# Kernel optimization log

Hardware: AMD Instinct MI355X
Metric: run time of the kernel (lower is better)

The kernel has to match this reference:

```python
import jax, jax.numpy as jnp
import numpy as np

N_NODES = 100000
N_EDGES = 1600000
NFEAT = 256
NHID = 128


def _l2_normalize(v, eps=1e-12):
    return v / (jnp.linalg.norm(v) + eps)


def setup_inputs() -> dict:
    key = jax.random.key(0)
    k1, k2, k3, k4 = jax.random.split(key, 4)
    x = jax.random.normal(k1, (N_NODES, NFEAT), dtype=jnp.float32)
    edge_index = jax.random.randint(k2, (2, N_EDGES), 0, N_NODES, dtype=jnp.int64)
    # GCNConv weight (glorot-ish scale), spectral-normalized at forward time
    W = jax.random.normal(k3, (NFEAT, NHID), dtype=jnp.float32) * 0.05
    bias = jnp.zeros((NHID,), dtype=jnp.float32)
    prelu_a = jnp.full((1,), 0.25, dtype=jnp.float32)  # nn.PReLU default slope
    u = _l2_normalize(jax.random.normal(k4, (NFEAT,), dtype=jnp.float32))
    return {"x": x, "edge_index": edge_index, "W": W, "bias": bias,
            "prelu_a": prelu_a, "u": u}


def reference(x, edge_index, W, bias, prelu_a, u):
    # --- spectral_norm: one power iteration (torch default n_power_iterations=1) ---
    v = _l2_normalize(W.T @ u)          # [NHID]
    u2 = _l2_normalize(W @ v)           # [NFEAT]
    sigma = u2 @ (W @ v)
    W_sn = W / sigma

    # --- GCNConv: linear transform, add self-loops, sym-normalize, scatter-add ---
    xw = x @ W_sn                       # [N, NHID]
    n = x.shape[0]
    loops = jnp.arange(n, dtype=edge_index.dtype)
    row = jnp.concatenate([edge_index[0], loops])  # sources
    col = jnp.concatenate([edge_index[1], loops])  # targets
    ones = jnp.ones(row.shape[0], dtype=x.dtype)
    deg = jax.ops.segment_sum(ones, col, num_segments=n)
    dinv = jnp.where(deg > 0, deg ** -0.5, 0.0)
    norm = dinv[row] * dinv[col]        # [E+N]
    msgs = norm[:, None] * xw[row]      # gather at sources
    out = jax.ops.segment_sum(msgs, col, num_segments=n) + bias

    # --- PReLU ---
    return jnp.where(out > 0, out, prelu_a * out)
```

## Files before the change

### kernel.cpp

```cpp
#include <hip/hip_runtime.h>

#define NFEAT 256
#define NHID  128

#define NBK   391
#define EPB   4096
#define NBLK  391

typedef __bf16 bf16x8 __attribute__((ext_vector_type(8)));
typedef __bf16 bf16x4 __attribute__((ext_vector_type(4)));
typedef float  f32x4  __attribute__((ext_vector_type(4)));

__global__ __launch_bounds__(256) void sigma_kernel(const float* __restrict__ W,
                                                    const float* __restrict__ u,
                                                    float* __restrict__ scal) {
    __shared__ float v[NHID];
    __shared__ float red[256];
    int tid = threadIdx.x;

    float t = 0.f;
    if (tid < NHID) {
        for (int i = 0; i < NFEAT; ++i) t += W[i * NHID + tid] * u[i];
    }
    red[tid] = (tid < NHID) ? t * t : 0.f;
    __syncthreads();
    for (int s = 128; s > 0; s >>= 1) {
        if (tid < s) red[tid] += red[tid + s];
        __syncthreads();
    }
    float nv = sqrtf(red[0]);
    float inv_nv = 1.f / (nv + 1e-12f);
    __syncthreads();
    if (tid < NHID) v[tid] = t * inv_nv;
    __syncthreads();

    float wv = 0.f;
    for (int j = 0; j < NHID; ++j) wv += W[tid * NHID + j] * v[j];
    red[tid] = wv * wv;
    __syncthreads();
    for (int s = 128; s > 0; s >>= 1) {
        if (tid < s) red[tid] += red[tid + s];
        __syncthreads();
    }
    if (tid == 0) {
        float n2  = red[0];
        float nwv = sqrtf(n2);
        float sigma = n2 / (nwv + 1e-12f);
        scal[0] = 1.f / sigma;
    }
}

__global__ __launch_bounds__(256) void wt_kernel(const float* __restrict__ W,
                                                 const float* __restrict__ scal,
                                                 __bf16* __restrict__ WT) {
    int idx = blockIdx.x * 256 + threadIdx.x;
    int c = idx >> 8;
    int r = idx & 255;
    WT[c * NFEAT + r] = (__bf16)(W[r * NHID + c] * scal[0]);
}

__global__ __launch_bounds__(256) void hist_kernel(const int* __restrict__ ecol,
                                                   int* __restrict__ blkhist, int E) {
    __shared__ int hist[NBK];
    int tid = threadIdx.x, b = blockIdx.x;
    for (int k = tid; k < NBK; k += 256) hist[k] = 0;
    __syncthreads();
    int e0 = b * EPB;
#pragma unroll
    for (int j = 0; j < 16; ++j) {
        int idx = e0 + j * 256 + tid;
        if (idx < E) atomicAdd(&hist[ecol[idx] >> 8], 1);
    }
    __syncthreads();
    for (int k = tid; k < NBK; k += 256) blkhist[k * NBLK + b] = hist[k];
}

__global__ __launch_bounds__(256) void scan_rows_kernel(int* __restrict__ blkhist,
                                                        int* __restrict__ btot) {
    int k = blockIdx.x * 4 + (threadIdx.x >> 6);
    int lane = threadIdx.x & 63;
    if (k >= NBK) return;
    int carry = 0;
    for (int c0 = 0; c0 < NBLK; c0 += 64) {
        int b = c0 + lane;
        int v = (b < NBLK) ? blkhist[k * NBLK + b] : 0;
        int orig = v;
#pragma unroll
        for (int d = 1; d < 64; d <<= 1) {
            int t = __shfl_up(v, (unsigned)d, 64);
            if (lane >= d) v += t;
        }
        if (b < NBLK) blkhist[k * NBLK + b] = carry + v - orig;
        carry += __shfl(v, 63, 64);
    }
    if (lane == 0) btot[k] = carry;
}

__global__ __launch_bounds__(512) void scan_buckets_kernel(const int* __restrict__ btot,
                                                           int* __restrict__ bbase) {
    __shared__ int s[512];
    int tid = threadIdx.x;
    int v = (tid < NBK) ? btot[tid] : 0;
    s[tid] = v;
    __syncthreads();
    int val = v;
    for (int off = 1; off < 512; off <<= 1) {
        int t = (tid >= off) ? s[tid - off] : 0;
        __syncthreads();
        val += t;
        s[tid] = val;
        __syncthreads();
    }
    if (tid <= NBK) bbase[tid] = val - v;
}

__global__ __launch_bounds__(512) void coarse_scatter_kernel(const int* __restrict__ erow,
                                                             const int* __restrict__ ecol,
                                                             const int* __restrict__ blkhist,
                                                             const int* __restrict__ bbase,
                                                             unsigned int* __restrict__ rbuf,
                                                             int E) {
    __shared__ unsigned int rec[EPB];
    __shared__ unsigned short bk[EPB];
    __shared__ int hist[NBK], sc[512], lbase[NBK], lfill[NBK], gb[NBK];
    int tid = threadIdx.x, b = blockIdx.x;
    for (int k = tid; k < NBK; k += 512) { hist[k] = 0; lfill[k] = 0; }
    __syncthreads();
    int e0 = b * EPB;
    unsigned int rv[8];
    int kv[8];
#pragma unroll
    for (int j = 0; j < 8; ++j) {
        int idx = e0 + j * 512 + tid;
        if (idx < E) {
            int c = ecol[idx];
            int s = erow[idx];
            int k = c >> 8;
            kv[j] = k;
            rv[j] = ((unsigned int)(c & 255) << 24) | (unsigned int)s;
            atomicAdd(&hist[k], 1);
        } else kv[j] = -1;
    }
    __syncthreads();
    int hv = (tid < NBK) ? hist[tid] : 0;
    sc[tid] = hv;
    __syncthreads();
    int val = hv;
    for (int off = 1; off < 512; off <<= 1) {
        int t = (tid >= off) ? sc[tid - off] : 0;
        __syncthreads();
        val += t;
        sc[tid] = val;
        __syncthreads();
    }
    if (tid < NBK) {
        lbase[tid] = val - hv;
        gb[tid] = bbase[tid] + blkhist[tid * NBLK + b];
    }
    __syncthreads();
#pragma unroll
    for (int j = 0; j < 8; ++j) {
        if (kv[j] >= 0) {
            int p = lbase[kv[j]] + atomicAdd(&lfill[kv[j]], 1);
            rec[p] = rv[j];
            bk[p] = (unsigned short)kv[j];
        }
    }
    __syncthreads();
    int nval = E - e0;
    if (nval > EPB) nval = EPB;
    for (int p = tid; p < nval; p += 512) {
        int k = bk[p];
        rbuf[gb[k] + (p - lbase[k])] = rec[p];
    }
}

__global__ __launch_bounds__(256) void fine_kernel(const unsigned int* __restrict__ rbuf,
                                                   const int* __restrict__ bbase,
                                                   int* __restrict__ base_g,
                                                   int* __restrict__ cnt_g,
                                                   float* __restrict__ dinv,
                                                   int* __restrict__ ebuf, int n) {
    __shared__ int cnt[256], lb[256], lf[256], sc[256];
    int tid = threadIdx.x, k = blockIdx.x;
    int seg0 = bbase[k], seg1 = bbase[k + 1];
    cnt[tid] = 0;
    lf[tid] = 0;
    __syncthreads();
    for (int j = seg0 + tid; j < seg1; j += 256)
        atomicAdd(&cnt[rbuf[j] >> 24], 1);
    __syncthreads();
    int cv = cnt[tid];
    sc[tid] = cv;
    __syncthreads();
    int val = cv;
    for (int off = 1; off < 256; off <<= 1) {
        int t = (tid >= off) ? sc[tid - off] : 0;
        __syncthreads();
        val += t;
        sc[tid] = val;
        __syncthreads();
    }
    lb[tid] = val - cv;
    __syncthreads();
    int node = k * 256 + tid;
    if (node < n) {
        base_g[node] = seg0 + lb[tid];
        cnt_g[node] = cv;
        dinv[node] = rsqrtf((float)cv + 1.f);
    }
    for (int j = seg0 + tid; j < seg1; j += 256) {
        unsigned int r = rbuf[j];
        int dl = r >> 24;
        int p = seg0 + lb[dl] + atomicAdd(&lf[dl], 1);
        ebuf[p] = (int)(r & 0xFFFFFFu);
    }
}

__global__ __launch_bounds__(256) void gemm_mfma_kernel(const float* __restrict__ x,
                                                        const __bf16* __restrict__ WT,
                                                        const float* __restrict__ dinv,
                                                        __bf16* __restrict__ xwb, int nn) {
    __shared__ float xs[2][64][64];

    int tid  = threadIdx.x;
    int lane = tid & 63;
    int w    = tid >> 6;
    int rfrag = lane & 15;
    int kg    = lane >> 4;
    int row0 = blockIdx.x * 64;

    int p16  = lane & 15;
    int rsub = lane >> 4;

    int crow0 = (w & 1) * 32 + rfrag;
    int col0  = (w >> 1) * 64;
    int r0 = row0 + crow0;
    int r1 = r0 + 16;
    const __bf16* wb = WT + (size_t)(col0 + rfrag) * NFEAT + kg * 8;
    int cr7 = crow0 & 7;

    f32x4 acc0[4] = {};
    f32x4 acc1[4] = {};

    auto STAGE = [&](int buf, int c) {
#pragma unroll
        for (int j = 0; j < 4; ++j) {
            int rloc = w * 16 + j * 4 + rsub;
            int grow = row0 + rloc;
            if (grow >= nn) grow = nn - 1;
            const float* src = x + (size_t)grow * NFEAT + c * 64 + ((p16 ^ (grow & 7)) << 2);
            __builtin_amdgcn_global_load_lds(
                (const __attribute__((address_space(1))) void*)src,
                (__attribute__((address_space(3))) void*)&xs[buf][w * 16 + j * 4][0],
                16, 0, 0);
        }
    };

    bf16x8 Bf[2][4];
    auto BLOAD = [&](int c) {
#pragma unroll
        for (int ks = 0; ks < 2; ++ks)
#pragma unroll
            for (int nt = 0; nt < 4; ++nt)
                Bf[ks][nt] = *(const bf16x8*)(wb + (size_t)nt * 16 * NFEAT + c * 64 + ks * 32);
    };

    auto MFMA_CHUNK = [&](int buf) {
#pragma unroll
        for (int ks = 0; ks < 2; ++ks) {
            int sA = kg * 2 + ks * 8;
            float4 a0lo = *(const float4*)&xs[buf][crow0][((sA) ^ cr7) * 4];
            float4 a0hi = *(const float4*)&xs[buf][crow0][((sA + 1) ^ cr7) * 4];
            float4 a1lo = *(const float4*)&xs[buf][crow0 + 16][((sA) ^ cr7) * 4];
            float4 a1hi = *(const float4*)&xs[buf][crow0 + 16][((sA + 1) ^ cr7) * 4];
            bf16x8 af0, af1;
            af0[0] = (__bf16)a0lo.x; af0[1] = (__bf16)a0lo.y;
            af0[2] = (__bf16)a0lo.z; af0[3] = (__bf16)a0lo.w;
            af0[4] = (__bf16)a0hi.x; af0[5] = (__bf16)a0hi.y;
            af0[6] = (__bf16)a0hi.z; af0[7] = (__bf16)a0hi.w;
            af1[0] = (__bf16)a1lo.x; af1[1] = (__bf16)a1lo.y;
            af1[2] = (__bf16)a1lo.z; af1[3] = (__bf16)a1lo.w;
            af1[4] = (__bf16)a1hi.x; af1[5] = (__bf16)a1hi.y;
            af1[6] = (__bf16)a1hi.z; af1[7] = (__bf16)a1hi.w;
#pragma unroll
            for (int nt = 0; nt < 4; ++nt) {
                acc0[nt] = __builtin_amdgcn_mfma_f32_16x16x32_bf16(Bf[ks][nt], af0, acc0[nt], 0, 0, 0);
                acc1[nt] = __builtin_amdgcn_mfma_f32_16x16x32_bf16(Bf[ks][nt], af1, acc1[nt], 0, 0, 0);
            }
        }
    };

#define DRAIN_BAR() do { \
        asm volatile("s_waitcnt vmcnt(0)" ::: "memory"); \
        __builtin_amdgcn_s_barrier(); } while (0)

    STAGE(0, 0);
    DRAIN_BAR();

    BLOAD(0);
    __builtin_amdgcn_sched_barrier(0);
    STAGE(1, 1);
    __builtin_amdgcn_sched_barrier(0);
    MFMA_CHUNK(0);
    DRAIN_BAR();

    BLOAD(1);
    __builtin_amdgcn_sched_barrier(0);
    STAGE(0, 2);
    __builtin_amdgcn_sched_barrier(0);
    MFMA_CHUNK(1);
    DRAIN_BAR();

    BLOAD(2);
    __builtin_amdgcn_sched_barrier(0);
    STAGE(1, 3);
    __builtin_amdgcn_sched_barrier(0);
    MFMA_CHUNK(0);
    DRAIN_BAR();

    BLOAD(3);
    MFMA_CHUNK(1);
#undef DRAIN_BAR

    if (r0 < nn) {
        float d = dinv[r0];
        __bf16* orow = xwb + (size_t)r0 * NHID + col0 + kg * 4;
#pragma unroll
        for (int nt = 0; nt < 4; ++nt) {
            bf16x4 v;
            v[0] = (__bf16)(acc0[nt][0] * d);
            v[1] = (__bf16)(acc0[nt][1] * d);
            v[2] = (__bf16)(acc0[nt][2] * d);
            v[3] = (__bf16)(acc0[nt][3] * d);
            *(bf16x4*)&orow[nt * 16] = v;
        }
    }
    if (r1 < nn) {
        float d = dinv[r1];
        __bf16* orow = xwb + (size_t)r1 * NHID + col0 + kg * 4;
#pragma unroll
        for (int nt = 0; nt < 4; ++nt) {
            bf16x4 v;
            v[0] = (__bf16)(acc1[nt][0] * d);
            v[1] = (__bf16)(acc1[nt][1] * d);
            v[2] = (__bf16)(acc1[nt][2] * d);
            v[3] = (__bf16)(acc1[nt][3] * d);
            *(bf16x4*)&orow[nt * 16] = v;
        }
    }
}

__global__ __launch_bounds__(256) void gather_kernel(const uint4* __restrict__ xb4,
                                                     const int* __restrict__ base,
                                                     const int* __restrict__ cnt,
                                                     const int* __restrict__ ebuf,
                                                     const float* __restrict__ dinv,
                                                     const float* __restrict__ bias,
                                                     const float* __restrict__ pa,
                                                     float* __restrict__ out, int n) {
    int tid = threadIdx.x;
    int sub = tid & 15;
    int node = (blockIdx.x * 256 + tid) >> 4;
    if (node >= n) return;

    int b = base[node];
    int deg = cnt[node];

    uint4 s0 = xb4[(size_t)node * 16 + sub];
    float a0 = __uint_as_float(s0.x << 16);
    float a1 = __uint_as_float(s0.x & 0xffff0000u);
    float a2 = __uint_as_float(s0.y << 16);
    float a3 = __uint_as_float(s0.y & 0xffff0000u);
    float a4 = __uint_as_float(s0.z << 16);
    float a5 = __uint_as_float(s0.z & 0xffff0000u);
    float a6 = __uint_as_float(s0.w << 16);
    float a7 = __uint_as_float(s0.w & 0xffff0000u);

    int k = 0;
    for (; k + 4 <= deg; k += 4) {
        int r0 = ebuf[b + k + 0];
        int r1 = ebuf[b + k + 1];
        int r2 = ebuf[b + k + 2];
        int r3 = ebuf[b + k + 3];
        uint4 v0 = xb4[(size_t)r0 * 16 + sub];
        uint4 v1 = xb4[(size_t)r1 * 16 + sub];
        uint4 v2 = xb4[(size_t)r2 * 16 + sub];
        uint4 v3 = xb4[(size_t)r3 * 16 + sub];
        a0 += __uint_as_float(v0.x << 16) + __uint_as_float(v1.x << 16)
            + __uint_as_float(v2.x << 16) + __uint_as_float(v3.x << 16);
        a1 += __uint_as_float(v0.x & 0xffff0000u) + __uint_as_float(v1.x & 0xffff0000u)
            + __uint_as_float(v2.x & 0xffff0000u) + __uint_as_float(v3.x & 0xffff0000u);
        a2 += __uint_as_float(v0.y << 16) + __uint_as_float(v1.y << 16)
            + __uint_as_float(v2.y << 16) + __uint_as_float(v3.y << 16);
        a3 += __uint_as_float(v0.y & 0xffff0000u) + __uint_as_float(v1.y & 0xffff0000u)
            + __uint_as_float(v2.y & 0xffff0000u) + __uint_as_float(v3.y & 0xffff0000u);
        a4 += __uint_as_float(v0.z << 16) + __uint_as_float(v1.z << 16)
            + __uint_as_float(v2.z << 16) + __uint_as_float(v3.z << 16);
        a5 += __uint_as_float(v0.z & 0xffff0000u) + __uint_as_float(v1.z & 0xffff0000u)
            + __uint_as_float(v2.z & 0xffff0000u) + __uint_as_float(v3.z & 0xffff0000u);
        a6 += __uint_as_float(v0.w << 16) + __uint_as_float(v1.w << 16)
            + __uint_as_float(v2.w << 16) + __uint_as_float(v3.w << 16);
        a7 += __uint_as_float(v0.w & 0xffff0000u) + __uint_as_float(v1.w & 0xffff0000u)
            + __uint_as_float(v2.w & 0xffff0000u) + __uint_as_float(v3.w & 0xffff0000u);
    }
    for (; k < deg; ++k) {
        int r = ebuf[b + k];
        uint4 v = xb4[(size_t)r * 16 + sub];
        a0 += __uint_as_float(v.x << 16);
        a1 += __uint_as_float(v.x & 0xffff0000u);
        a2 += __uint_as_float(v.y << 16);
        a3 += __uint_as_float(v.y & 0xffff0000u);
        a4 += __uint_as_float(v.z << 16);
        a5 += __uint_as_float(v.z & 0xffff0000u);
        a6 += __uint_as_float(v.w << 16);
        a7 += __uint_as_float(v.w & 0xffff0000u);
    }

    float s = dinv[node];
    float alpha = pa[0];
    const float4* bb4 = (const float4*)bias;
    float4 b0 = bb4[sub * 2], b1 = bb4[sub * 2 + 1];
    float o0 = s * a0 + b0.x;
    float o1 = s * a1 + b0.y;
    float o2 = s * a2 + b0.z;
    float o3 = s * a3 + b0.w;
    float o4 = s * a4 + b1.x;
    float o5 = s * a5 + b1.y;
    float o6 = s * a6 + b1.z;
    float o7 = s * a7 + b1.w;
    o0 = o0 > 0.f ? o0 : alpha * o0;
    o1 = o1 > 0.f ? o1 : alpha * o1;
    o2 = o2 > 0.f ? o2 : alpha * o2;
    o3 = o3 > 0.f ? o3 : alpha * o3;
    o4 = o4 > 0.f ? o4 : alpha * o4;
    o5 = o5 > 0.f ? o5 : alpha * o5;
    o6 = o6 > 0.f ? o6 : alpha * o6;
    o7 = o7 > 0.f ? o7 : alpha * o7;
    float4* orow = (float4*)out + (size_t)node * 32 + sub * 2;
    orow[0] = make_float4(o0, o1, o2, o3);
    orow[1] = make_float4(o4, o5, o6, o7);
}

extern "C" void kernel_launch(void* const* d_in, const int* in_sizes, int n_in,
                              void* d_out, int out_size, void* d_ws, size_t ws_size,
                              hipStream_t stream) {
    const float* x    = (const float*)d_in[0];
    const int*   ei   = (const int*)d_in[1];
    const float* W    = (const float*)d_in[2];
    const float* bias = (const float*)d_in[3];
    const float* pa   = (const float*)d_in[4];
    const float* u    = (const float*)d_in[5];

    int n = in_sizes[0] / NFEAT;
    int e = in_sizes[1] / 2;
    const int* erow = ei;
    const int* ecol = ei + e;

    float* out = (float*)d_out;
    char* ws = (char*)d_ws;
    float*        scal   = (float*)(ws);
    int*          btot   = (int*)  (ws + 0x0001000);
    int*          bbase  = (int*)  (ws + 0x0002000);
    __bf16*       WT     = (__bf16*)(ws + 0x0010000);
    int*          base_g = (int*)  (ws + 0x0100000);
    int*          cnt_g  = (int*)  (ws + 0x0200000);
    float*        dinv   = (float*)(ws + 0x0300000);
    int*          blkhist= (int*)  (ws + 0x0400000);
    unsigned int* rbuf   = (unsigned int*)(ws + 0x0500000);
    int*          ebuf   = (int*)  (ws + 0x0C00000);
    __bf16*       xwb    = (__bf16*)(ws + 0x1300000);

    sigma_kernel<<<1, 256, 0, stream>>>(W, u, scal);
    wt_kernel<<<(NFEAT * NHID) / 256, 256, 0, stream>>>(W, scal, WT);

    hist_kernel<<<NBLK, 256, 0, stream>>>(ecol, blkhist, e);
    scan_rows_kernel<<<(NBK + 3) / 4, 256, 0, stream>>>(blkhist, btot);
    scan_buckets_kernel<<<1, 512, 0, stream>>>(btot, bbase);
    coarse_scatter_kernel<<<NBLK, 512, 0, stream>>>(erow, ecol, blkhist, bbase, rbuf, e);
    fine_kernel<<<NBK, 256, 0, stream>>>(rbuf, bbase, base_g, cnt_g, dinv, ebuf, n);

    gemm_mfma_kernel<<<(n + 63) / 64, 256, 0, stream>>>(x, WT, dinv, xwb, n);

    long long gunits = (long long)n * 16;
    gather_kernel<<<(int)((gunits + 255) / 256), 256, 0, stream>>>(
        (const uint4*)xwb, base_g, cnt_g, ebuf, dinv, bias, pa, out, n);
}
```

Before: 157.3 us.

## Fuse GEMM with coarse edge scatter and use fixed-stride atomic bucket segments

Removes the global histogram, row scan and bucket scan kernels by giving each bucket a fixed-capacity segment (SEGW) whose fill level is claimed with a global atomicAdd. The coarse scatter now runs in the same launch as the MFMA GEMM, with blocks split by index, so the two independent stages overlap. Because dinv is no longer known when the GEMM runs, the per-source degree scaling moves into the gather, which adds an extra dinv load per edge. The fixed segment size assumes no bucket holds more than SEGW edges, which holds only for roughly uniform column distributions, and edge order within a bucket becomes nondeterministic.

New measurement: 146.1 us. 1.08x faster.

```diff
diff --git a/kernel.cpp b/kernel.cpp
--- a/kernel.cpp
+++ b/kernel.cpp
@@ -6,6 +6,7 @@
 #define NBK   391
 #define EPB   4096
 #define NBLK  391
+#define SEGW  4608
 
 typedef __bf16 bf16x8 __attribute__((ext_vector_type(8)));
 typedef __bf16 bf16x4 __attribute__((ext_vector_type(4)));
@@ -13,10 +14,14 @@
 
 __global__ __launch_bounds__(256) void sigma_kernel(const float* __restrict__ W,
                                                     const float* __restrict__ u,
-                                                    float* __restrict__ scal) {
+                                                    float* __restrict__ scal,
+                                                    int* __restrict__ bucket_fill) {
     __shared__ float v[NHID];
     __shared__ float red[256];
     int tid = threadIdx.x;
+
+    if (tid < NBK) bucket_fill[tid] = 0;
+    if (tid + 256 < NBK) bucket_fill[tid + 256] = 0;
 
     float t = 0.f;
     if (tid < NHID) {
@@ -59,79 +64,164 @@
     WT[c * NFEAT + r] = (__bf16)(W[r * NHID + c] * scal[0]);
 }
 
-__global__ __launch_bounds__(256) void hist_kernel(const int* __restrict__ ecol,
-                                                   int* __restrict__ blkhist, int E) {
-    __shared__ int hist[NBK];
-    int tid = threadIdx.x, b = blockIdx.x;
-    for (int k = tid; k < NBK; k += 256) hist[k] = 0;
-    __syncthreads();
+__global__ __launch_bounds__(256) void fused_kernel(const float* __restrict__ x,
+                                                    const __bf16* __restrict__ WT,
+                                                    __bf16* __restrict__ xwb,
+                                                    const int* __restrict__ erow,
+                                                    const int* __restrict__ ecol,
+                                                    int* __restrict__ bucket_fill,
+                                                    unsigned int* __restrict__ rbuf,
+                                                    int nn, int E, int ngemm) {
+    __shared__ __attribute__((aligned(16))) char sbuf[32768];
+
+    int tid  = threadIdx.x;
+
+    if ((int)blockIdx.x < ngemm) {
+        float (*xs)[64][64] = (float (*)[64][64])sbuf;
+
+        int lane = tid & 63;
+        int w    = tid >> 6;
+        int rfrag = lane & 15;
+        int kg    = lane >> 4;
+        int row0 = blockIdx.x * 64;
+
+        int p16  = lane & 15;
+        int rsub = lane >> 4;
+
+        int crow0 = (w & 1) * 32 + rfrag;
+        int col0  = (w >> 1) * 64;
+        int r0 = row0 + crow0;
+        int r1 = r0 + 16;
+        const __bf16* wb = WT + (size_t)(col0 + rfrag) * NFEAT + kg * 8;
+        int cr7 = crow0 & 7;
+
+        f32x4 acc0[4] = {};
+        f32x4 acc1[4] = {};
+
+        auto STAGE = [&](int buf, int c) {
+#pragma unroll
+            for (int j = 0; j < 4; ++j) {
+                int rloc = w * 16 + j * 4 + rsub;
+                int grow = row0 + rloc;
+                if (grow >= nn) grow = nn - 1;
+                const float* src = x + (size_t)grow * NFEAT + c * 64 + ((p16 ^ (grow & 7)) << 2);
+                __builtin_amdgcn_global_load_lds(
+                    (const __attribute__((address_space(1))) void*)src,
+                    (__attribute__((address_space(3))) void*)&xs[buf][w * 16 + j * 4][0],
+                    16, 0, 0);
+            }
+        };
+
+        bf16x8 Bf[2][4];
+        auto BLOAD = [&](int c) {
+#pragma unroll
+            for (int ks = 0; ks < 2; ++ks)
+#pragma unroll
+                for (int nt = 0; nt < 4; ++nt)
+                    Bf[ks][nt] = *(const bf16x8*)(wb + (size_t)nt * 16 * NFEAT + c * 64 + ks * 32);
+        };
+
+        auto MFMA_CHUNK = [&](int buf) {
+#pragma unroll
+            for (int ks = 0; ks < 2; ++ks) {
+                int sA = kg * 2 + ks * 8;
+                float4 a0lo = *(const float4*)&xs[buf][crow0][((sA) ^ cr7) * 4];
+                float4 a0hi = *(const float4*)&xs[buf][crow0][((sA + 1) ^ cr7) * 4];
+                float4 a1lo = *(const float4*)&xs[buf][crow0 + 16][((sA) ^ cr7) * 4];
+                float4 a1hi = *(const float4*)&xs[buf][crow0 + 16][((sA + 1) ^ cr7) * 4];
+                bf16x8 af0, af1;
+                af0[0] = (__bf16)a0lo.x; af0[1] = (__bf16)a0lo.y;
+                af0[2] = (__bf16)a0lo.z; af0[3] = (__bf16)a0lo.w;
+                af0[4] = (__bf16)a0hi.x; af0[5] = (__bf16)a0hi.y;
+                af0[6] = (__bf16)a0hi.z; af0[7] = (__bf16)a0hi.w;
+                af1[0] = (__bf16)a1lo.x; af1[1] = (__bf16)a1lo.y;
+                af1[2] = (__bf16)a1lo.z; af1[3] = (__bf16)a1lo.w;
+                af1[4] = (__bf16)a1hi.x; af1[5] = (__bf16)a1hi.y;
+                af1[6] = (__bf16)a1hi.z; af1[7] = (__bf16)a1hi.w;
+#pragma unroll
+                for (int nt = 0; nt < 4; ++nt) {
+                    acc0[nt] = __builtin_amdgcn_mfma_f32_16x16x32_bf16(Bf[ks][nt], af0, acc0[nt], 0, 0, 0);
+                    acc1[nt] = __builtin_amdgcn_mfma_f32_16x16x32_bf16(Bf[ks][nt], af1, acc1[nt], 0, 0, 0);
+                }
+            }
+        };
+
+#define DRAIN_BAR() do { \
+            asm volatile("s_waitcnt vmcnt(0)" ::: "memory"); \
+            __builtin_amdgcn_s_barrier(); } while (0)
+
+        STAGE(0, 0);
+        DRAIN_BAR();
+
+        BLOAD(0);
+        __builtin_amdgcn_sched_barrier(0);
+        STAGE(1, 1);
+        __builtin_amdgcn_sched_barrier(0);
+        MFMA_CHUNK(0);
+        DRAIN_BAR();
+
+        BLOAD(1);
+        __builtin_amdgcn_sched_barrier(0);
+        STAGE(0, 2);
+        __builtin_amdgcn_sched_barrier(0);
+        MFMA_CHUNK(1);
+        DRAIN_BAR();
+
+        BLOAD(2);
+        __builtin_amdgcn_sched_barrier(0);
+        STAGE(1, 3);
+        __builtin_amdgcn_sched_barrier(0);
+        MFMA_CHUNK(0);
+        DRAIN_BAR();
+
+        BLOAD(3);
+        MFMA_CHUNK(1);
+#undef DRAIN_BAR
+
+        if (r0 < nn) {
+            __bf16* orow = xwb + (size_t)r0 * NHID + col0 + kg * 4;
+#pragma unroll
+            for (int nt = 0; nt < 4; ++nt) {
+                bf16x4 v;
+                v[0] = (__bf16)acc0[nt][0];
+                v[1] = (__bf16)acc0[nt][1];
+                v[2] = (__bf16)acc0[nt][2];
+                v[3] = (__bf16)acc0[nt][3];
+                *(bf16x4*)&orow[nt * 16] = v;
+            }
+        }
+        if (r1 < nn) {
+            __bf16* orow = xwb + (size_t)r1 * NHID + col0 + kg * 4;
+#pragma unroll
+            for (int nt = 0; nt < 4; ++nt) {
+                bf16x4 v;
+                v[0] = (__bf16)acc1[nt][0];
+                v[1] = (__bf16)acc1[nt][1];
+                v[2] = (__bf16)acc1[nt][2];
+                v[3] = (__bf16)acc1[nt][3];
+                *(bf16x4*)&orow[nt * 16] = v;
+            }
+        }
+        return;
+    }
+
+    unsigned int*   rec   = (unsigned int*)sbuf;
+    unsigned short* bkk   = (unsigned short*)(sbuf + 16384);
+    int*            hist  = (int*)(sbuf + 24576);
+    int*            lbase = (int*)(sbuf + 24576 + 1564);
+    int*            lfill = (int*)(sbuf + 24576 + 3128);
+    int*            gb    = (int*)(sbuf + 24576 + 4692);
+
+    int b = blockIdx.x - ngemm;
+    for (int k = tid; k < NBK; k += 256) { hist[k] = 0; lfill[k] = 0; }
+    __syncthreads();
+
     int e0 = b * EPB;
+    unsigned int rv[16];
+    int kv[16];
 #pragma unroll
     for (int j = 0; j < 16; ++j) {
         int idx = e0 + j * 256 + tid;
-        if (idx < E) atomicAdd(&hist[ecol[idx] >> 8], 1);
-    }
-    __syncthreads();
-    for (int k = tid; k < NBK; k += 256) blkhist[k * NBLK + b] = hist[k];
-}
-
-__global__ __launch_bounds__(256) void scan_rows_kernel(int* __restrict__ blkhist,
-                                                        int* __restrict__ btot) {
-    int k = blockIdx.x * 4 + (threadIdx.x >> 6);
-    int lane = threadIdx.x & 63;
-    if (k >= NBK) return;
-    int carry = 0;
-    for (int c0 = 0; c0 < NBLK; c0 += 64) {
-        int b = c0 + lane;
-        int v = (b < NBLK) ? blkhist[k * NBLK + b] : 0;
-        int orig = v;
-#pragma unroll
-        for (int d = 1; d < 64; d <<= 1) {
-            int t = __shfl_up(v, (unsigned)d, 64);
-            if (lane >= d) v += t;
-        }
-        if (b < NBLK) blkhist[k * NBLK + b] = carry + v - orig;
-        carry += __shfl(v, 63, 64);
-    }
-    if (lane == 0) btot[k] = carry;
-}
-
-__global__ __launch_bounds__(512) void scan_buckets_kernel(const int* __restrict__ btot,
-                                                           int* __restrict__ bbase) {
-    __shared__ int s[512];
-    int tid = threadIdx.x;
-    int v = (tid < NBK) ? btot[tid] : 0;
-    s[tid] = v;
-    __syncthreads();
-    int val = v;
-    for (int off = 1; off < 512; off <<= 1) {
-        int t = (tid >= off) ? s[tid - off] : 0;
-        __syncthreads();
-        val += t;
-        s[tid] = val;
-        __syncthreads();
-    }
-    if (tid <= NBK) bbase[tid] = val - v;
-}
-
-__global__ __launch_bounds__(512) void coarse_scatter_kernel(const int* __restrict__ erow,
-                                                             const int* __restrict__ ecol,
-                                                             const int* __restrict__ blkhist,
-                                                             const int* __restrict__ bbase,
-                                                             unsigned int* __restrict__ rbuf,
-                                                             int E) {
-    __shared__ unsigned int rec[EPB];
-    __shared__ unsigned short bk[EPB];
-    __shared__ int hist[NBK], sc[512], lbase[NBK], lfill[NBK], gb[NBK];
-    int tid = threadIdx.x, b = blockIdx.x;
-    for (int k = tid; k < NBK; k += 512) { hist[k] = 0; lfill[k] = 0; }
-    __syncthreads();
-    int e0 = b * EPB;
-    unsigned int rv[8];
-    int kv[8];
-#pragma unroll
-    for (int j = 0; j < 8; ++j) {
-        int idx = e0 + j * 512 + tid;
         if (idx < E) {
             int c = ecol[idx];
             int s = erow[idx];
@@ -142,48 +232,56 @@
         } else kv[j] = -1;
     }
     __syncthreads();
-    int hv = (tid < NBK) ? hist[tid] : 0;
-    sc[tid] = hv;
-    __syncthreads();
-    int val = hv;
-    for (int off = 1; off < 512; off <<= 1) {
-        int t = (tid >= off) ? sc[tid - off] : 0;
-        __syncthreads();
-        val += t;
-        sc[tid] = val;
-        __syncthreads();
-    }
-    if (tid < NBK) {
-        lbase[tid] = val - hv;
-        gb[tid] = bbase[tid] + blkhist[tid * NBLK + b];
-    }
-    __syncthreads();
-#pragma unroll
-    for (int j = 0; j < 8; ++j) {
+
+    if (tid < 64) {
+        int carry = 0;
+        for (int c0 = 0; c0 < NBK; c0 += 64) {
+            int i = c0 + tid;
+            int vv = (i < NBK) ? hist[i] : 0;
+            int orig = vv;
+#pragma unroll
+            for (int d = 1; d < 64; d <<= 1) {
+                int t = __shfl_up(vv, (unsigned)d, 64);
+                if (tid >= d) vv += t;
+            }
+            if (i < NBK) lbase[i] = carry + vv - orig;
+            carry += __shfl(vv, 63, 64);
+        }
+    }
+    __syncthreads();
+
+    if (tid < NBK) gb[tid] = tid * SEGW + atomicAdd(&bucket_fill[tid], hist[tid]);
+    if (tid + 256 < NBK) gb[tid + 256] = (tid + 256) * SEGW
+                                       + atomicAdd(&bucket_fill[tid + 256], hist[tid + 256]);
+    __syncthreads();
+
+#pragma unroll
+    for (int j = 0; j < 16; ++j) {
         if (kv[j] >= 0) {
             int p = lbase[kv[j]] + atomicAdd(&lfill[kv[j]], 1);
             rec[p] = rv[j];
-            bk[p] = (unsigned short)kv[j];
+            bkk[p] = (unsigned short)kv[j];
         }
     }
     __syncthreads();
+
     int nval = E - e0;
     if (nval > EPB) nval = EPB;
-    for (int p = tid; p < nval; p += 512) {
-        int k = bk[p];
+    for (int p = tid; p < nval; p += 256) {
+        int k = bkk[p];
         rbuf[gb[k] + (p - lbase[k])] = rec[p];
     }
 }
 
 __global__ __launch_bounds__(256) void fine_kernel(const unsigned int* __restrict__ rbuf,
-                                                   const int* __restrict__ bbase,
+                                                   const int* __restrict__ bucket_fill,
                                                    int* __restrict__ base_g,
                                                    int* __restrict__ cnt_g,
                                                    float* __restrict__ dinv,
                                                    int* __restrict__ ebuf, int n) {
     __shared__ int cnt[256], lb[256], lf[256], sc[256];
     int tid = threadIdx.x, k = blockIdx.x;
-    int seg0 = bbase[k], seg1 = bbase[k + 1];
+    int seg0 = k * SEGW, seg1 = seg0 + bucket_fill[k];
     cnt[tid] = 0;
     lf[tid] = 0;
     __syncthreads();
@@ -214,140 +312,6 @@
         int dl = r >> 24;
         int p = seg0 + lb[dl] + atomicAdd(&lf[dl], 1);
         ebuf[p] = (int)(r & 0xFFFFFFu);
-    }
-}
-
-__global__ __launch_bounds__(256) void gemm_mfma_kernel(const float* __restrict__ x,
-                                                        const __bf16* __restrict__ WT,
-                                                        const float* __restrict__ dinv,
-                                                        __bf16* __restrict__ xwb, int nn) {
-    __shared__ float xs[2][64][64];
-
-    int tid  = threadIdx.x;
-    int lane = tid & 63;
-    int w    = tid >> 6;
-    int rfrag = lane & 15;
-    int kg    = lane >> 4;
-    int row0 = blockIdx.x * 64;
-
-    int p16  = lane & 15;
-    int rsub = lane >> 4;
-
-    int crow0 = (w & 1) * 32 + rfrag;
-    int col0  = (w >> 1) * 64;
-    int r0 = row0 + crow0;
-    int r1 = r0 + 16;
-    const __bf16* wb = WT + (size_t)(col0 + rfrag) * NFEAT + kg * 8;
-    int cr7 = crow0 & 7;
-
-    f32x4 acc0[4] = {};
-    f32x4 acc1[4] = {};
-
-    auto STAGE = [&](int buf, int c) {
-#pragma unroll
-        for (int j = 0; j < 4; ++j) {
-            int rloc = w * 16 + j * 4 + rsub;
-            int grow = row0 + rloc;
-            if (grow >= nn) grow = nn - 1;
-            const float* src = x + (size_t)grow * NFEAT + c * 64 + ((p16 ^ (grow & 7)) << 2);
-            __builtin_amdgcn_global_load_lds(
-                (const __attribute__((address_space(1))) void*)src,
-                (__attribute__((address_space(3))) void*)&xs[buf][w * 16 + j * 4][0],
-                16, 0, 0);
-        }
-    };
-
-    bf16x8 Bf[2][4];
-    auto BLOAD = [&](int c) {
-#pragma unroll
-        for (int ks = 0; ks < 2; ++ks)
-#pragma unroll
-            for (int nt = 0; nt < 4; ++nt)
-                Bf[ks][nt] = *(const bf16x8*)(wb + (size_t)nt * 16 * NFEAT + c * 64 + ks * 32);
-    };
-
-    auto MFMA_CHUNK = [&](int buf) {
-#pragma unroll
-        for (int ks = 0; ks < 2; ++ks) {
-            int sA = kg * 2 + ks * 8;
-            float4 a0lo = *(const float4*)&xs[buf][crow0][((sA) ^ cr7) * 4];
-            float4 a0hi = *(const float4*)&xs[buf][crow0][((sA + 1) ^ cr7) * 4];
-            float4 a1lo = *(const float4*)&xs[buf][crow0 + 16][((sA) ^ cr7) * 4];
-            float4 a1hi = *(const float4*)&xs[buf][crow0 + 16][((sA + 1) ^ cr7) * 4];
-            bf16x8 af0, af1;
-            af0[0] = (__bf16)a0lo.x; af0[1] = (__bf16)a0lo.y;
-            af0[2] = (__bf16)a0lo.z; af0[3] = (__bf16)a0lo.w;
-            af0[4] = (__bf16)a0hi.x; af0[5] = (__bf16)a0hi.y;
-            af0[6] = (__bf16)a0hi.z; af0[7] = (__bf16)a0hi.w;
-            af1[0] = (__bf16)a1lo.x; af1[1] = (__bf16)a1lo.y;
-            af1[2] = (__bf16)a1lo.z; af1[3] = (__bf16)a1lo.w;
-            af1[4] = (__bf16)a1hi.x; af1[5] = (__bf16)a1hi.y;
-            af1[6] = (__bf16)a1hi.z; af1[7] = (__bf16)a1hi.w;
-#pragma unroll
-            for (int nt = 0; nt < 4; ++nt) {
-                acc0[nt] = __builtin_amdgcn_mfma_f32_16x16x32_bf16(Bf[ks][nt], af0, acc0[nt], 0, 0, 0);
-                acc1[nt] = __builtin_amdgcn_mfma_f32_16x16x32_bf16(Bf[ks][nt], af1, acc1[nt], 0, 0, 0);
-            }
-        }
-    };
-
-#define DRAIN_BAR() do { \
-        asm volatile("s_waitcnt vmcnt(0)" ::: "memory"); \
-        __builtin_amdgcn_s_barrier(); } while (0)
-
-    STAGE(0, 0);
-    DRAIN_BAR();
-
-    BLOAD(0);
-    __builtin_amdgcn_sched_barrier(0);
-    STAGE(1, 1);
-    __builtin_amdgcn_sched_barrier(0);
-    MFMA_CHUNK(0);
-    DRAIN_BAR();
-
-    BLOAD(1);
-    __builtin_amdgcn_sched_barrier(0);
-    STAGE(0, 2);
-    __builtin_amdgcn_sched_barrier(0);
-    MFMA_CHUNK(1);
-    DRAIN_BAR();
-
-    BLOAD(2);
-    __builtin_amdgcn_sched_barrier(0);
-    STAGE(1, 3);
-    __builtin_amdgcn_sched_barrier(0);
-    MFMA_CHUNK(0);
-    DRAIN_BAR();
-
-    BLOAD(3);
-    MFMA_CHUNK(1);
-#undef DRAIN_BAR
-
-    if (r0 < nn) {
-        float d = dinv[r0];
-        __bf16* orow = xwb + (size_t)r0 * NHID + col0 + kg * 4;
-#pragma unroll
-        for (int nt = 0; nt < 4; ++nt) {
-            bf16x4 v;
-            v[0] = (__bf16)(acc0[nt][0] * d);
-            v[1] = (__bf16)(acc0[nt][1] * d);
-            v[2] = (__bf16)(acc0[nt][2] * d);
-            v[3] = (__bf16)(acc0[nt][3] * d);
-            *(bf16x4*)&orow[nt * 16] = v;
-        }
-    }
-    if (r1 < nn) {
-        float d = dinv[r1];
-        __bf16* orow = xwb + (size_t)r1 * NHID + col0 + kg * 4;
-#pragma unroll
-        for (int nt = 0; nt < 4; ++nt) {
-            bf16x4 v;
-            v[0] = (__bf16)(acc1[nt][0] * d);
-            v[1] = (__bf16)(acc1[nt][1] * d);
-            v[2] = (__bf16)(acc1[nt][2] * d);
-            v[3] = (__bf16)(acc1[nt][3] * d);
-            *(bf16x4*)&orow[nt * 16] = v;
-        }
     }
 }
 
@@ -366,16 +330,17 @@
 
     int b = base[node];
     int deg = cnt[node];
+    float dn = dinv[node];
 
     uint4 s0 = xb4[(size_t)node * 16 + sub];
-    float a0 = __uint_as_float(s0.x << 16);
-    float a1 = __uint_as_float(s0.x & 0xffff0000u);
-    float a2 = __uint_as_float(s0.y << 16);
-    float a3 = __uint_as_float(s0.y & 0xffff0000u);
-    float a4 = __uint_as_float(s0.z << 16);
-    float a5 = __uint_as_float(s0.z & 0xffff0000u);
-    float a6 = __uint_as_float(s0.w << 16);
-    float a7 = __uint_as_float(s0.w & 0xffff0000u);
+    float a0 = dn * __uint_as_float(s0.x << 16);
+    float a1 = dn * __uint_as_float(s0.x & 0xffff0000u);
+    float a2 = dn * __uint_as_float(s0.y << 16);
+    float a3 = dn * __uint_as_float(s0.y & 0xffff0000u);
+    float a4 = dn * __uint_as_float(s0.z << 16);
+    float a5 = dn * __uint_as_float(s0.z & 0xffff0000u);
+    float a6 = dn * __uint_as_float(s0.w << 16);
+    float a7 = dn * __uint_as_float(s0.w & 0xffff0000u);
 
     int k = 0;
     for (; k + 4 <= deg; k += 4) {
@@ -383,52 +348,53 @@
         int r1 = ebuf[b + k + 1];
         int r2 = ebuf[b + k + 2];
         int r3 = ebuf[b + k + 3];
+        float d0 = dinv[r0], d1 = dinv[r1], d2 = dinv[r2], d3 = dinv[r3];
         uint4 v0 = xb4[(size_t)r0 * 16 + sub];
         uint4 v1 = xb4[(size_t)r1 * 16 + sub];
         uint4 v2 = xb4[(size_t)r2 * 16 + sub];
         uint4 v3 = xb4[(size_t)r3 * 16 + sub];
-        a0 += __uint_as_float(v0.x << 16) + __uint_as_float(v1.x << 16)
-            + __uint_as_float(v2.x << 16) + __uint_as_float(v3.x << 16);
-        a1 += __uint_as_float(v0.x & 0xffff0000u) + __uint_as_float(v1.x & 0xffff0000u)
-            + __uint_as_float(v2.x & 0xffff0000u) + __uint_as_float(v3.x & 0xffff0000u);
-        a2 += __uint_as_float(v0.y << 16) + __uint_as_float(v1.y << 16)
-            + __uint_as_float(v2.y << 16) + __uint_as_float(v3.y << 16);
-        a3 += __uint_as_float(v0.y & 0xffff0000u) + __uint_as_float(v1.y & 0xffff0000u)
-            + __uint_as_float(v2.y & 0xffff0000u) + __uint_as_float(v3.y & 0xffff0000u);
-        a4 += __uint_as_float(v0.z << 16) + __uint_as_float(v1.z << 16)
-            + __uint_as_float(v2.z << 16) + __uint_as_float(v3.z << 16);
-        a5 += __uint_as_float(v0.z & 0xffff0000u) + __uint_as_float(v1.z & 0xffff0000u)
-            + __uint_as_float(v2.z & 0xffff0000u) + __uint_as_float(v3.z & 0xffff0000u);
-        a6 += __uint_as_float(v0.w << 16) + __uint_as_float(v1.w << 16)
-            + __uint_as_float(v2.w << 16) + __uint_as_float(v3.w << 16);
-        a7 += __uint_as_float(v0.w & 0xffff0000u) + __uint_as_float(v1.w & 0xffff0000u)
-            + __uint_as_float(v2.w & 0xffff0000u) + __uint_as_float(v3.w & 0xffff0000u);
+        a0 += d0 * __uint_as_float(v0.x << 16) + d1 * __uint_as_float(v1.x << 16)
+            + d2 * __uint_as_float(v2.x << 16) + d3 * __uint_as_float(v3.x << 16);
+        a1 += d0 * __uint_as_float(v0.x & 0xffff0000u) + d1 * __uint_as_float(v1.x & 0xffff0000u)
+            + d2 * __uint_as_float(v2.x & 0xffff0000u) + d3 * __uint_as_float(v3.x & 0xffff0000u);
+        a2 += d0 * __uint_as_float(v0.y << 16) + d1 * __uint_as_float(v1.y << 16)
+            + d2 * __uint_as_float(v2.y << 16) + d3 * __uint_as_float(v3.y << 16);
+        a3 += d0 * __uint_as_float(v0.y & 0xffff0000u) + d1 * __uint_as_float(v1.y & 0xffff0000u)
+            + d2 * __uint_as_float(v2.y & 0xffff0000u) + d3 * __uint_as_float(v3.y & 0xffff0000u);
+        a4 += d0 * __uint_as_float(v0.z << 16) + d1 * __uint_as_float(v1.z << 16)
+            + d2 * __uint_as_float(v2.z << 16) + d3 * __uint_as_float(v3.z << 16);
+        a5 += d0 * __uint_as_float(v0.z & 0xffff0000u) + d1 * __uint_as_float(v1.z & 0xffff0000u)
+            + d2 * __uint_as_float(v2.z & 0xffff0000u) + d3 * __uint_as_float(v3.z & 0xffff0000u);
+        a6 += d0 * __uint_as_float(v0.w << 16) + d1 * __uint_as_float(v1.w << 16)
+            + d2 * __uint_as_float(v2.w << 16) + d3 * __uint_as_float(v3.w << 16);
+        a7 += d0 * __uint_as_float(v0.w & 0xffff0000u) + d1 * __uint_as_float(v1.w & 0xffff0000u)
+            + d2 * __uint_as_float(v2.w & 0xffff0000u) + d3 * __uint_as_float(v3.w & 0xffff0000u);
     }
     for (; k < deg; ++k) {
         int r = ebuf[b + k];
+        float d = dinv[r];
         uint4 v = xb4[(size_t)r * 16 + sub];
-        a0 += __uint_as_float(v.x << 16);
-        a1 += __uint_as_float(v.x & 0xffff0000u);
-        a2 += __uint_as_float(v.y << 16);
-        a3 += __uint_as_float(v.y & 0xffff0000u);
-        a4 += __uint_as_float(v.z << 16);
-        a5 += __uint_as_float(v.z & 0xffff0000u);
-        a6 += __uint_as_float(v.w << 16);
-        a7 += __uint_as_float(v.w & 0xffff0000u);
-    }
-
-    float s = dinv[node];
+        a0 += d * __uint_as_float(v.x << 16);
+        a1 += d * __uint_as_float(v.x & 0xffff0000u);
+        a2 += d * __uint_as_float(v.y << 16);
+        a3 += d * __uint_as_float(v.y & 0xffff0000u);
+        a4 += d * __uint_as_float(v.z << 16);
+        a5 += d * __uint_as_float(v.z & 0xffff0000u);
+        a6 += d * __uint_as_float(v.w << 16);
+        a7 += d * __uint_as_float(v.w & 0xffff0000u);
+    }
+
     float alpha = pa[0];
     const float4* bb4 = (const float4*)bias;
     float4 b0 = bb4[sub * 2], b1 = bb4[sub * 2 + 1];
-    float o0 = s * a0 + b0.x;
-    float o1 = s * a1 + b0.y;
-    float o2 = s * a2 + b0.z;
-    float o3 = s * a3 + b0.w;
-    float o4 = s * a4 + b1.x;
-    float o5 = s * a5 + b1.y;
-    float o6 = s * a6 + b1.z;
-    float o7 = s * a7 + b1.w;
+    float o0 = dn * a0 + b0.x;
+    float o1 = dn * a1 + b0.y;
+    float o2 = dn * a2 + b0.z;
+    float o3 = dn * a3 + b0.w;
+    float o4 = dn * a4 + b1.x;
+    float o5 = dn * a5 + b1.y;
+    float o6 = dn * a6 + b1.z;
+    float o7 = dn * a7 + b1.w;
     o0 = o0 > 0.f ? o0 : alpha * o0;
     o1 = o1 > 0.f ? o1 : alpha * o1;
     o2 = o2 > 0.f ? o2 : alpha * o2;
@@ -460,27 +426,24 @@
     float* out = (float*)d_out;
     char* ws = (char*)d_ws;
     float*        scal   = (float*)(ws);
-    int*          btot   = (int*)  (ws + 0x0001000);
-    int*          bbase  = (int*)  (ws + 0x0002000);
+    int*          bfill  = (int*)  (ws + 0x0002000);
     __bf16*       WT     = (__bf16*)(ws + 0x0010000);
     int*          base_g = (int*)  (ws + 0x0100000);
     int*          cnt_g  = (int*)  (ws + 0x0200000);
     float*        dinv   = (float*)(ws + 0x0300000);
-    int*          blkhist= (int*)  (ws + 0x0400000);
     unsigned int* rbuf   = (unsigned int*)(ws + 0x0500000);
     int*          ebuf   = (int*)  (ws + 0x0C00000);
     __bf16*       xwb    = (__bf16*)(ws + 0x1300000);
 
-    sigma_kernel<<<1, 256, 0, stream>>>(W, u, scal);
+    int ngemm = (n + 63) / 64;
+
+    sigma_kernel<<<1, 256, 0, stream>>>(W, u, scal, bfill);
     wt_kernel<<<(NFEAT * NHID) / 256, 256, 0, stream>>>(W, scal, WT);
 
-    hist_kernel<<<NBLK, 256, 0, stream>>>(ecol, blkhist, e);
-    scan_rows_kernel<<<(NBK + 3) / 4, 256, 0, stream>>>(blkhist, btot);
-    scan_buckets_kernel<<<1, 512, 0, stream>>>(btot, bbase);
-    coarse_scatter_kernel<<<NBLK, 512, 0, stream>>>(erow, ecol, blkhist, bbase, rbuf, e);
-    fine_kernel<<<NBK, 256, 0, stream>>>(rbuf, bbase, base_g, cnt_g, dinv, ebuf, n);
-
-    gemm_mfma_kernel<<<(n + 63) / 64, 256, 0, stream>>>(x, WT, dinv, xwb, n);
+    fused_kernel<<<ngemm + NBLK, 256, 0, stream>>>(x, WT, xwb, erow, ecol,
+                                                   bfill, rbuf, n, e, ngemm);
+
+    fine_kernel<<<NBK, 256, 0, stream>>>(rbuf, bfill, base_g, cnt_g, dinv, ebuf, n);
 
     long long gunits = (long long)n * 16;
     gather_kernel<<<(int)((gunits + 255) / 256), 256, 0, stream>>>(
```
